# Performance work log

Measured on AMD Instinct MI355X. Metric: run time of the kernel, lower is better.

The kernel has to match this reference:

```python
import jax, jax.numpy as jnp
import numpy as np
import math

# --- module config (init_kwargs) ---
DES_R = 2.0
RAD_N, AZI_N, ELE_N = 5, 30, 15
TWO_PI = 2.0 * math.pi
PI = math.pi


def setup_inputs() -> dict:
    key = jax.random.key(0)
    points = jax.random.normal(key, (16, 65536, 3), dtype=jnp.float32)
    return {"points": points}


def _xyz2spherical(pts):
    x, y, z = pts[..., 0], pts[..., 1], pts[..., 2]
    r = jnp.sqrt(x * x + y * y + z * z)
    azi = jnp.arctan2(y, x)
    azi = jnp.where(azi < 0, azi + TWO_PI, azi)  # [0, 2pi)
    ele = jnp.arccos(jnp.clip(z / jnp.maximum(r, 1e-12), -1.0, 1.0))  # [0, pi]
    return r, azi, ele


def _two_nearest(d, step):
    # two smallest distances per point along last axis -> interp weights 1 - d/step
    neg, idx = jax.lax.top_k(-d, 2)
    w = 1.0 + neg / step
    return w, idx


def _voxelize(points):
    B, N, _ = points.shape
    r, azi, ele = _xyz2spherical(points)

    # ---- radial axis: centers at (j+0.5)*step, boundary half-bin clamping ----
    tr = DES_R / RAD_N
    sr = tr / 2
    cr = (jnp.arange(RAD_N, dtype=points.dtype) + 0.5) * tr
    dr = jnp.abs(r[..., None] - cr)  # [B,N,RAD_N]
    low = (r < sr)[..., None]
    dr = jnp.where(low & (dr <= sr), 0.0, dr)               # nearest bin -> weight 1
    dr = jnp.where(low & (dr > tr) & (dr <= tr + sr), tr, dr)  # 2nd bin -> weight 0
    high = ((r > DES_R - sr) & (r <= DES_R))[..., None]
    dr = jnp.where(high & (dr > tr) & (dr <= tr + sr), tr, dr)
    wr, ir = _two_nearest(dr, tr)
    wr = jnp.where((r > DES_R)[..., None], 0.0, wr)  # cull points outside sphere

    # ---- azimuth axis: circular distance (== torch wraparound fixups) ----
    ta = TWO_PI / AZI_N
    ca = (jnp.arange(AZI_N, dtype=points.dtype) + 0.5) * ta
    da = jnp.abs(azi[..., None] - ca)
    da = jnp.minimum(da, TWO_PI - da)
    wa, ia = _two_nearest(da, ta)
    wa = jnp.where((azi > TWO_PI)[..., None], 0.0, wa)

    # ---- elevation axis: boundary half-bin clamping on both ends ----
    te = PI / ELE_N
    se = te / 2
    ce = (jnp.arange(ELE_N, dtype=points.dtype) + 0.5) * te
    de = jnp.abs(ele[..., None] - ce)
    lo = (ele < se)[..., None]
    de = jnp.where(lo & (de <= se), 0.0, de)
    de = jnp.where(lo & (de > te) & (de <= te + se), te, de)
    hi = ((ele > PI - se) & (ele <= PI))[..., None]
    de = jnp.where(hi & (de <= 0.75 * te), 0.0, de)
    de = jnp.where(hi & (de > te) & (de <= te + se), te, de)
    we, ie = _two_nearest(de, te)
    we = jnp.where((ele > PI)[..., None], 0.0, we)

    # ---- trilinear weights for the 8 (r,a,e) neighbor combos; scatter-add ----
    w8 = (wr[:, :, :, None, None] * wa[:, :, None, :, None] * we[:, :, None, None, :]).reshape(B, N, 8)
    f8 = ((ir[:, :, :, None, None] * AZI_N + ia[:, :, None, :, None]) * ELE_N + ie[:, :, None, None, :]).reshape(B, N, 8)
    f8 = f8 + jnp.arange(B, dtype=f8.dtype)[:, None, None] * (RAD_N * AZI_N * ELE_N)
    hist = jax.ops.segment_sum(w8.reshape(-1), f8.reshape(-1), num_segments=B * RAD_N * AZI_N * ELE_N)
    return hist.reshape(B, 1, RAD_N, AZI_N, ELE_N)


def reference(points):
    return _voxelize(points)
```

## Files before the change

kernel.cpp:

```cpp
#include <hip/hip_runtime.h>
#include <math.h>


constexpr int RAD_N = 5, AZI_N = 30, ELE_N = 15;
constexpr int BINS  = RAD_N * AZI_N * ELE_N;
constexpr int BLOCK = 512;
constexpr int PPT   = 2;
constexpr int PPB   = BLOCK * PPT;
constexpr float FX_SCALE = 2097152.0f;
constexpr float FX_INV   = 1.0f / 2097152.0f;

__device__ __forceinline__ float fast_atan2_02pi(float y, float x) {
    const float PI_F     = 3.14159265358979f;
    const float TWO_PI_F = 6.28318530717959f;
    const float HALF_PI  = 1.57079632679490f;
    float ax = fabsf(x), ay = fabsf(y);
    float mx = fmaxf(ax, ay), mn = fminf(ax, ay);
    float t  = mn * __builtin_amdgcn_rcpf(mx);
    float t2 = t * t;
    float p = -0.01172120f;
    p = __builtin_fmaf(p, t2,  0.05265332f);
    p = __builtin_fmaf(p, t2, -0.11643287f);
    p = __builtin_fmaf(p, t2,  0.19354346f);
    p = __builtin_fmaf(p, t2, -0.33262347f);
    p = __builtin_fmaf(p, t2,  0.99997726f);
    float th = t * p;
    th = (ay > ax) ? (HALF_PI - th) : th;
    th = (x < 0.0f) ? (PI_F - th) : th;
    th = (y < 0.0f) ? (TWO_PI_F - th) : th;
    return th;
}

__device__ __forceinline__ float fast_acos(float x) {
    const float PI_F = 3.14159265358979f;
    float a = fabsf(x);
    float p = -0.0012624911f;
    p = __builtin_fmaf(p, a,  0.0066700901f);
    p = __builtin_fmaf(p, a, -0.0170881256f);
    p = __builtin_fmaf(p, a,  0.0308918810f);
    p = __builtin_fmaf(p, a, -0.0501743046f);
    p = __builtin_fmaf(p, a,  0.0889789874f);
    p = __builtin_fmaf(p, a, -0.2145988016f);
    p = __builtin_fmaf(p, a,  1.5707963050f);
    float s = __builtin_amdgcn_sqrtf(1.0f - a);
    float r = s * p;
    return (x < 0.0f) ? (PI_F - r) : r;
}

__device__ __forceinline__ unsigned to_fx(float w) {
    float v = __builtin_fmaf(w, FX_SCALE, 0.5f);
    return (unsigned)fmaxf(v, 0.0f);
}

__device__ __forceinline__ void process_point(float x, float y, float z,
                                              unsigned* hist) {
    const float TWO_PI_F = (float)(6.283185307179586);
    const float PI_F     = (float)(3.141592653589793);
    const float tr       = (float)(2.0 / 5.0);
    const float sr       = (float)(2.0 / 5.0 / 2.0);
    const float tr_p_sr  = (float)(0.4 + 0.2);
    const float rhi_lo   = (float)(2.0 - 0.2);
    const float DES_R_F  = 2.0f;
    const float ta       = (float)(6.283185307179586 / 30.0);
    const float te       = (float)(3.141592653589793 / 15.0);
    const float se       = (float)(3.141592653589793 / 30.0);
    const float te_p_se  = (float)(3.141592653589793 / 15.0 + 3.141592653589793 / 30.0);
    const float te075    = (float)(0.75 * (3.141592653589793 / 15.0));
    const float pi_m_se  = (float)(3.141592653589793 - 3.141592653589793 / 30.0);
    const float inv_tr   = (float)(5.0 / 2.0);
    const float inv_ta   = (float)(30.0 / 6.283185307179586);
    const float inv_te   = (float)(15.0 / 3.141592653589793);

    float r = __builtin_amdgcn_sqrtf(x * x + y * y + z * z);
    if (r > DES_R_F) return;

    float azi = fast_atan2_02pi(y, x);
    float cz = z * __builtin_amdgcn_rcpf(fmaxf(r, 1e-12f));
    cz = fminf(fmaxf(cz, -1.0f), 1.0f);
    float ele = fast_acos(cz);

    int ra = (int)(r * inv_tr);
    if (ra > RAD_N - 1) ra = RAD_N - 1;
    float cra = ((float)ra + 0.5f) * tr;
    int rb = (r > cra) ? ra + 1 : ra - 1;
    rb = (rb < 0) ? 1 : ((rb > RAD_N - 1) ? RAD_N - 2 : rb);
    float dra = fabsf(r - cra);
    float drb = fabsf(r - ((float)rb + 0.5f) * tr);
    {
        bool lowR  = r < sr;
        bool highR = (r > rhi_lo);
        if (lowR) {
            dra = (dra <= sr) ? 0.0f : ((dra > tr && dra <= tr_p_sr) ? tr : dra);
            drb = (drb <= sr) ? 0.0f : ((drb > tr && drb <= tr_p_sr) ? tr : drb);
        }
        if (highR) {
            if (dra > tr && dra <= tr_p_sr) dra = tr;
            if (drb > tr && drb <= tr_p_sr) drb = tr;
        }
    }
    float wra = 1.0f - dra * inv_tr;
    float wrb = 1.0f - drb * inv_tr;

    int aa = (int)(azi * inv_ta);
    if (aa > AZI_N - 1) aa = AZI_N - 1;
    float caa = ((float)aa + 0.5f) * ta;
    int ab = (azi > caa) ? aa + 1 : aa - 1;
    ab = (ab < 0) ? AZI_N - 1 : ((ab > AZI_N - 1) ? 0 : ab);
    float daa = fabsf(azi - caa);
    daa = fminf(daa, TWO_PI_F - daa);
    float dab = fabsf(azi - ((float)ab + 0.5f) * ta);
    dab = fminf(dab, TWO_PI_F - dab);
    float waa = 1.0f - daa * inv_ta;
    float wab = 1.0f - dab * inv_ta;

    int ea = (int)(ele * inv_te);
    if (ea > ELE_N - 1) ea = ELE_N - 1;
    float cea = ((float)ea + 0.5f) * te;
    int eb = (ele > cea) ? ea + 1 : ea - 1;
    eb = (eb < 0) ? 1 : ((eb > ELE_N - 1) ? ELE_N - 2 : eb);
    float dea = fabsf(ele - cea);
    float deb = fabsf(ele - ((float)eb + 0.5f) * te);
    {
        bool lowE  = ele < se;
        bool highE = (ele > pi_m_se) && (ele <= PI_F);
        if (lowE) {
            dea = (dea <= se) ? 0.0f : ((dea > te && dea <= te_p_se) ? te : dea);
            deb = (deb <= se) ? 0.0f : ((deb > te && deb <= te_p_se) ? te : deb);
        }
        if (highE) {
            dea = (dea <= te075) ? 0.0f : ((dea > te && dea <= te_p_se) ? te : dea);
            deb = (deb <= te075) ? 0.0f : ((deb > te && deb <= te_p_se) ? te : deb);
        }
    }
    float wea = 1.0f - dea * inv_te;
    float web = 1.0f - deb * inv_te;

    int rbase_a = ra * (AZI_N * ELE_N), rbase_b = rb * (AZI_N * ELE_N);
    int abase_a = aa * ELE_N,           abase_b = ab * ELE_N;
    float w_aa = wra * waa, w_ab = wra * wab;
    float w_ba = wrb * waa, w_bb = wrb * wab;

    atomicAdd(&hist[rbase_a + abase_a + ea], to_fx(w_aa * wea));
    atomicAdd(&hist[rbase_a + abase_a + eb], to_fx(w_aa * web));
    atomicAdd(&hist[rbase_a + abase_b + ea], to_fx(w_ab * wea));
    atomicAdd(&hist[rbase_a + abase_b + eb], to_fx(w_ab * web));
    atomicAdd(&hist[rbase_b + abase_a + ea], to_fx(w_ba * wea));
    atomicAdd(&hist[rbase_b + abase_a + eb], to_fx(w_ba * web));
    atomicAdd(&hist[rbase_b + abase_b + ea], to_fx(w_bb * wea));
    atomicAdd(&hist[rbase_b + abase_b + eb], to_fx(w_bb * web));
}

__global__ __launch_bounds__(BLOCK) void voxel_store(
    const float* __restrict__ pts, unsigned* __restrict__ ws_u,
    int N, int blocksPerBatch)
{
    __shared__ unsigned hist[BINS];
    for (int j = threadIdx.x; j < BINS; j += BLOCK) hist[j] = 0u;
    __syncthreads();

    const int batch = blockIdx.x / blocksPerBatch;
    const int bib   = blockIdx.x % blocksPerBatch;
    const size_t batch_off = (size_t)batch * N;
    const int i0 = bib * PPB + (int)threadIdx.x * PPT;

    if (i0 + PPT <= N) {
        const float2* src = (const float2*)(pts + (batch_off + i0) * 3);
        float2 q0 = src[0];
        float2 q1 = src[1];
        float2 q2 = src[2];
        process_point(q0.x, q0.y, q1.x, hist);
        process_point(q1.y, q2.x, q2.y, hist);
    } else {
        for (int k = 0; k < PPT; ++k) {
            int i = i0 + k;
            if (i < N) {
                size_t p = (batch_off + i) * 3;
                process_point(pts[p], pts[p + 1], pts[p + 2], hist);
            }
        }
    }

    __syncthreads();
    unsigned* wb = ws_u + (size_t)blockIdx.x * BINS;
    for (int j = threadIdx.x; j < BINS; j += BLOCK) wb[j] = hist[j];
}

__global__ __launch_bounds__(256) void reduce_convert(
    const unsigned* __restrict__ ws_u, float* __restrict__ out,
    int blocksPerBatch, int total)
{
    int idx = blockIdx.x * 256 + (int)threadIdx.x;
    if (idx >= total) return;
    int batch = idx / BINS;
    int bin   = idx - batch * BINS;
    const unsigned* src = ws_u + (size_t)batch * blocksPerBatch * BINS + bin;
    unsigned s0 = 0u, s1 = 0u, s2 = 0u, s3 = 0u;
    int k = 0;
    for (; k + 3 < blocksPerBatch; k += 4) {
        unsigned a0 = src[(size_t)(k + 0) * BINS];
        unsigned a1 = src[(size_t)(k + 1) * BINS];
        unsigned a2 = src[(size_t)(k + 2) * BINS];
        unsigned a3 = src[(size_t)(k + 3) * BINS];
        s0 += a0; s1 += a1; s2 += a2; s3 += a3;
    }
    for (; k < blocksPerBatch; ++k) s0 += src[(size_t)k * BINS];
    out[idx] = (float)((s0 + s1) + (s2 + s3)) * FX_INV;
}

extern "C" void kernel_launch(void* const* d_in, const int* in_sizes, int n_in,
                              void* d_out, int out_size, void* d_ws, size_t ws_size,
                              hipStream_t stream) {
    const float* pts = (const float*)d_in[0];
    float* out = (float*)d_out;

    const int B = 16;
    int total = in_sizes[0] / 3;
    int N = total / B;
    int blocksPerBatch = (N + PPB - 1) / PPB;
    int grid = B * blocksPerBatch;

    unsigned* ws_u = (unsigned*)d_ws;
    voxel_store<<<dim3(grid), dim3(BLOCK), 0, stream>>>(pts, ws_u, N, blocksPerBatch);
    int rtotal = B * BINS;
    reduce_convert<<<dim3((rtotal + 255) / 256), dim3(256), 0, stream>>>(
        ws_u, out, blocksPerBatch, rtotal);
}
```

Baseline: 68.69 us.

## Pack adjacent elevation bins into 64-bit LDS atomics via split even/odd histograms

Each point's two elevation neighbours are always adjacent bins, so the eight 32-bit shared-memory atomics become four 64-bit atomics. Two shared histograms are kept, the odd one offset by one word, so every 64-bit add stays 8-byte aligned; they are summed when the block writes out. The boundary clamping branches are also wrapped in wave-uniform __any checks so most waves skip them. This halves LDS atomic count at the cost of doubled shared memory and relies on no carry crossing between the packed halves.

```diff
diff --git a/kernel.cpp b/kernel.cpp
--- a/kernel.cpp
+++ b/kernel.cpp
@@ -52,8 +52,16 @@
     return (unsigned)fmaxf(v, 0.0f);
 }
 
+__device__ __forceinline__ void emit_pair(unsigned* bufE, unsigned* bufO,
+                                          int idx, float flo, float fhi) {
+    unsigned long long v =
+        ((unsigned long long)to_fx(fhi) << 32) | (unsigned long long)to_fx(flo);
+    unsigned* base = (idx & 1) ? (bufO + 1) : bufE;
+    atomicAdd((unsigned long long*)(base + idx), v);
+}
+
 __device__ __forceinline__ void process_point(float x, float y, float z,
-                                              unsigned* hist) {
+                                              unsigned* bufE, unsigned* bufO) {
     const float TWO_PI_F = (float)(6.283185307179586);
     const float PI_F     = (float)(3.141592653589793);
     const float tr       = (float)(2.0 / 5.0);
@@ -89,9 +97,11 @@
     {
         bool lowR  = r < sr;
         bool highR = (r > rhi_lo);
-        if (lowR) {
-            dra = (dra <= sr) ? 0.0f : ((dra > tr && dra <= tr_p_sr) ? tr : dra);
-            drb = (drb <= sr) ? 0.0f : ((drb > tr && drb <= tr_p_sr) ? tr : drb);
+        if (__any(lowR)) {
+            if (lowR) {
+                dra = (dra <= sr) ? 0.0f : ((dra > tr && dra <= tr_p_sr) ? tr : dra);
+                drb = (drb <= sr) ? 0.0f : ((drb > tr && drb <= tr_p_sr) ? tr : drb);
+            }
         }
         if (highR) {
             if (dra > tr && dra <= tr_p_sr) dra = tr;
@@ -123,39 +133,44 @@
     {
         bool lowE  = ele < se;
         bool highE = (ele > pi_m_se) && (ele <= PI_F);
-        if (lowE) {
-            dea = (dea <= se) ? 0.0f : ((dea > te && dea <= te_p_se) ? te : dea);
-            deb = (deb <= se) ? 0.0f : ((deb > te && deb <= te_p_se) ? te : deb);
-        }
-        if (highE) {
-            dea = (dea <= te075) ? 0.0f : ((dea > te && dea <= te_p_se) ? te : dea);
-            deb = (deb <= te075) ? 0.0f : ((deb > te && deb <= te_p_se) ? te : deb);
+        if (__any(lowE)) {
+            if (lowE) {
+                dea = (dea <= se) ? 0.0f : ((dea > te && dea <= te_p_se) ? te : dea);
+                deb = (deb <= se) ? 0.0f : ((deb > te && deb <= te_p_se) ? te : deb);
+            }
+        }
+        if (__any(highE)) {
+            if (highE) {
+                dea = (dea <= te075) ? 0.0f : ((dea > te && dea <= te_p_se) ? te : dea);
+                deb = (deb <= te075) ? 0.0f : ((deb > te && deb <= te_p_se) ? te : deb);
+            }
         }
     }
     float wea = 1.0f - dea * inv_te;
     float web = 1.0f - deb * inv_te;
+
+    int elo   = (ea < eb) ? ea : eb;
+    float wlo = (ea < eb) ? wea : web;
+    float whi = (ea < eb) ? web : wea;
 
     int rbase_a = ra * (AZI_N * ELE_N), rbase_b = rb * (AZI_N * ELE_N);
     int abase_a = aa * ELE_N,           abase_b = ab * ELE_N;
     float w_aa = wra * waa, w_ab = wra * wab;
     float w_ba = wrb * waa, w_bb = wrb * wab;
 
-    atomicAdd(&hist[rbase_a + abase_a + ea], to_fx(w_aa * wea));
-    atomicAdd(&hist[rbase_a + abase_a + eb], to_fx(w_aa * web));
-    atomicAdd(&hist[rbase_a + abase_b + ea], to_fx(w_ab * wea));
-    atomicAdd(&hist[rbase_a + abase_b + eb], to_fx(w_ab * web));
-    atomicAdd(&hist[rbase_b + abase_a + ea], to_fx(w_ba * wea));
-    atomicAdd(&hist[rbase_b + abase_a + eb], to_fx(w_ba * web));
-    atomicAdd(&hist[rbase_b + abase_b + ea], to_fx(w_bb * wea));
-    atomicAdd(&hist[rbase_b + abase_b + eb], to_fx(w_bb * web));
+    emit_pair(bufE, bufO, rbase_a + abase_a + elo, w_aa * wlo, w_aa * whi);
+    emit_pair(bufE, bufO, rbase_a + abase_b + elo, w_ab * wlo, w_ab * whi);
+    emit_pair(bufE, bufO, rbase_b + abase_a + elo, w_ba * wlo, w_ba * whi);
+    emit_pair(bufE, bufO, rbase_b + abase_b + elo, w_bb * wlo, w_bb * whi);
 }
 
 __global__ __launch_bounds__(BLOCK) void voxel_store(
     const float* __restrict__ pts, unsigned* __restrict__ ws_u,
     int N, int blocksPerBatch)
 {
-    __shared__ unsigned hist[BINS];
-    for (int j = threadIdx.x; j < BINS; j += BLOCK) hist[j] = 0u;
+    __shared__ __align__(8) unsigned bufE[BINS + 2];
+    __shared__ __align__(8) unsigned bufO[BINS + 2];
+    for (int j = threadIdx.x; j < BINS + 2; j += BLOCK) { bufE[j] = 0u; bufO[j] = 0u; }
     __syncthreads();
 
     const int batch = blockIdx.x / blocksPerBatch;
@@ -168,21 +183,21 @@
         float2 q0 = src[0];
         float2 q1 = src[1];
         float2 q2 = src[2];
-        process_point(q0.x, q0.y, q1.x, hist);
-        process_point(q1.y, q2.x, q2.y, hist);
+        process_point(q0.x, q0.y, q1.x, bufE, bufO);
+        process_point(q1.y, q2.x, q2.y, bufE, bufO);
     } else {
         for (int k = 0; k < PPT; ++k) {
             int i = i0 + k;
             if (i < N) {
                 size_t p = (batch_off + i) * 3;
-                process_point(pts[p], pts[p + 1], pts[p + 2], hist);
+                process_point(pts[p], pts[p + 1], pts[p + 2], bufE, bufO);
             }
         }
     }
 
     __syncthreads();
     unsigned* wb = ws_u + (size_t)blockIdx.x * BINS;
-    for (int j = threadIdx.x; j < BINS; j += BLOCK) wb[j] = hist[j];
+    for (int j = threadIdx.x; j < BINS; j += BLOCK) wb[j] = bufE[j] + bufO[j + 1];
 }
 
 __global__ __launch_bounds__(256) void reduce_convert(
```

Measured after the change: 69.24 us. Within noise of the previous version (+0.8%).
